# Kernel tuning notes

Hardware: AMD Instinct MI355X
Metric: run time of the kernel (lower is better)

Reference implementation:

```python
import jax, jax.numpy as jnp
import numpy as np

N_NODES = 50000


def _relgraphconv(x, W, Wloop, b, src, dst, etypes, n_nodes):
    # DGL RelGraphConv (regularizer=None, self_loop=True, norm=None):
    # out[i] = sum over incoming edges (j->i, rel r) of W_r @ x[j]  +  W_loop @ x[i]  +  b
    # low-mem form: transform all nodes per relation, then gather per edge.
    h_rel = jnp.einsum('ni,rio->rno', x, W)          # [R, N, out]
    msg = h_rel[etypes, src]                          # [E, out]
    agg = jax.ops.segment_sum(msg, dst, num_segments=n_nodes)  # [N, out]
    return agg + x @ Wloop + b


def setup_inputs() -> dict:
    key = jax.random.key(0)
    ks = jax.random.split(key, 12)
    N, E, n_state = N_NODES, 800000, 128
    inp = {
        'x': jax.random.normal(ks[0], (N, n_state), dtype=jnp.float32),
        'src': jax.random.randint(ks[1], (E,), 0, N, dtype=jnp.int32),
        'dst': jax.random.randint(ks[2], (E,), 0, N, dtype=jnp.int32),
        'etypes': jax.random.randint(ks[3], (E,), 0, 2, dtype=jnp.int32),
        'cell_size': jax.random.randint(ks[4], (N,), 0, 8, dtype=jnp.int32),
        'max_size': jax.random.randint(ks[5], (N,), 0, 8, dtype=jnp.int32),
        'W1': jax.random.normal(ks[6], (2, n_state, 64), dtype=jnp.float32) * 0.05,
        'loop1': jax.random.normal(ks[7], (n_state, 64), dtype=jnp.float32) * 0.05,
        'b1': jnp.zeros((64,), dtype=jnp.float32),
        'W2': jax.random.normal(ks[8], (2, 64, 64), dtype=jnp.float32) * 0.05,
        'loop2': jax.random.normal(ks[9], (64, 64), dtype=jnp.float32) * 0.05,
        'b2': jnp.zeros((64,), dtype=jnp.float32),
        'W3': jax.random.normal(ks[10], (2, 64, 2), dtype=jnp.float32) * 0.05,
        'loop3': jax.random.normal(ks[11], (64, 2), dtype=jnp.float32) * 0.05,
        'b3': jnp.zeros((2,), dtype=jnp.float32),
    }
    return inp


def reference(x, src, dst, etypes, cell_size, max_size,
              W1, loop1, b1, W2, loop2, b2, W3, loop3, b3):
    N = x.shape[0]
    h = jax.nn.relu(_relgraphconv(x, W1, loop1, b1, src, dst, etypes, N))
    h = jax.nn.relu(_relgraphconv(h, W2, loop2, b2, src, dst, etypes, N))
    h = _relgraphconv(h, W3, loop3, b3, src, dst, etypes, N)   # [N, 2]
    # action mask: col 0 = cannot upsize, col 1 = cannot downsize
    upper = cell_size >= (max_size - 1)
    lower = cell_size == 0
    mask = jnp.stack([upper, lower], axis=1)                   # [N, 2] bool
    return jnp.where(mask, h.min() - 1.0, h)
```

## Files before the change

kernel.cpp:

```cpp
#include <hip/hip_runtime.h>


#define STRIDE 64

typedef unsigned short ushortT;
typedef __attribute__((ext_vector_type(8))) short short8;
typedef __attribute__((ext_vector_type(4))) float f32x4;

__device__ inline ushortT f2bf(float f) {
    union { float f; unsigned u; } v; v.f = f;
    unsigned r = v.u + 0x7FFFu + ((v.u >> 16) & 1u);
    return (ushortT)(r >> 16);
}
__device__ inline float bf2f(ushortT h) {
    union { unsigned u; float f; } v; v.u = ((unsigned)h) << 16;
    return v.f;
}

__device__ inline void atomicMinF(float* addr, float v) {
    if (v >= 0.f) atomicMin((int*)addr, __float_as_int(v));
    else          atomicMax((unsigned int*)addr, __float_as_uint(v));
}

__global__ __launch_bounds__(256) void pack_scatter_kernel(
    const float* __restrict__ W1, const float* __restrict__ loop1,
    const float* __restrict__ W2, const float* __restrict__ loop2,
    ushortT* __restrict__ BP1, ushortT* __restrict__ BP2,
    const int* __restrict__ src, const int* __restrict__ dst,
    const int* __restrict__ et, int* __restrict__ cnt, int* __restrict__ eidx,
    int N, int E) {
    if (blockIdx.x < 18) {
        int g = (int)blockIdx.x * 256 + (int)threadIdx.x;
        if (g < 3072) {
            int l = g & 63, ks = (g >> 6) & 3, ct = g >> 8;
            int c = ct * 16 + (l & 15);
            int mat = c >> 6, cc = c & 63;
            int kbase = ks * 32 + (l >> 4) * 8;
            ushortT* dstp = BP1 + (size_t)g * 8;
#pragma unroll
            for (int j = 0; j < 8; ++j) {
                int k = kbase + j;
                float v = (mat < 2) ? W1[((size_t)mat * 128 + k) * 64 + cc]
                                    : loop1[(size_t)k * 64 + cc];
                dstp[j] = f2bf(v);
            }
        } else {
            int s = g - 3072;
            int l = s & 63, ks = (s >> 6) & 1, ct = s >> 7;
            int c = ct * 16 + (l & 15);
            int mat = c >> 6, cc = c & 63;
            int kbase = ks * 32 + (l >> 4) * 8;
            ushortT* dstp = BP2 + (size_t)s * 8;
#pragma unroll
            for (int j = 0; j < 8; ++j) {
                int k = kbase + j;
                float v = (mat < 2) ? W2[((size_t)mat * 64 + k) * 64 + cc]
                                    : loop2[(size_t)k * 64 + cc];
                dstp[j] = f2bf(v);
            }
        }
        return;
    }
    int e0 = ((int)blockIdx.x - 18) * 1024 + (int)threadIdx.x;
    int e1 = e0 + 256, e2 = e0 + 512, e3 = e0 + 768;
    bool a0 = e0 < E, a1 = e1 < E, a2 = e2 < E, a3 = e3 < E;
    int d0 = a0 ? dst[e0] : 0, d1 = a1 ? dst[e1] : 0;
    int d2 = a2 ? dst[e2] : 0, d3 = a3 ? dst[e3] : 0;
    int v0 = a0 ? (et[e0] * N + src[e0]) : 0;
    int v1 = a1 ? (et[e1] * N + src[e1]) : 0;
    int v2 = a2 ? (et[e2] * N + src[e2]) : 0;
    int v3 = a3 ? (et[e3] * N + src[e3]) : 0;
    int p0 = 0, p1 = 0, p2 = 0, p3 = 0;
    if (a0) p0 = atomicAdd(&cnt[d0], 1);
    if (a1) p1 = atomicAdd(&cnt[d1], 1);
    if (a2) p2 = atomicAdd(&cnt[d2], 1);
    if (a3) p3 = atomicAdd(&cnt[d3], 1);
    if (a0 && p0 < STRIDE) eidx[(size_t)d0 * STRIDE + p0] = v0;
    if (a1 && p1 < STRIDE) eidx[(size_t)d1 * STRIDE + p1] = v1;
    if (a2 && p2 < STRIDE) eidx[(size_t)d2 * STRIDE + p2] = v2;
    if (a3 && p3 < STRIDE) eidx[(size_t)d3 * STRIDE + p3] = v3;
}

__global__ __launch_bounds__(256) void gemm1_mfma(
    const float* __restrict__ x, const ushortT* __restrict__ BP1,
    const float* __restrict__ b1,
    ushortT* __restrict__ hrelb, ushortT* __restrict__ H1b, int N) {
    const int w = (int)threadIdx.x >> 6, lane = (int)threadIdx.x & 63;
    const int rowbase = ((int)blockIdx.x * 4 + w) * 16;
    const int m = lane & 15, quad = lane >> 4;
    const int nclamp = min(rowbase + m, N - 1);

    short8 a[4];
    const float* xp = x + (size_t)nclamp * 128 + quad * 8;
#pragma unroll
    for (int ks = 0; ks < 4; ++ks) {
        float4 g0 = *(const float4*)(xp + ks * 32);
        float4 g1 = *(const float4*)(xp + ks * 32 + 4);
        a[ks][0] = (short)f2bf(g0.x); a[ks][1] = (short)f2bf(g0.y);
        a[ks][2] = (short)f2bf(g0.z); a[ks][3] = (short)f2bf(g0.w);
        a[ks][4] = (short)f2bf(g1.x); a[ks][5] = (short)f2bf(g1.y);
        a[ks][6] = (short)f2bf(g1.z); a[ks][7] = (short)f2bf(g1.w);
    }

    f32x4 acc[12];
#pragma unroll
    for (int ct = 0; ct < 12; ++ct) acc[ct] = (f32x4){0.f, 0.f, 0.f, 0.f};

#pragma unroll
    for (int ks = 0; ks < 4; ++ks) {
#pragma unroll
        for (int ct = 0; ct < 12; ++ct) {
            short8 b = *(const short8*)&BP1[((size_t)(ct * 4 + ks) * 64 + lane) * 8];
            acc[ct] = __builtin_amdgcn_mfma_f32_16x16x32_bf16(a[ks], b, acc[ct], 0, 0, 0);
        }
    }

    const int node0 = rowbase + quad * 4;
#pragma unroll
    for (int ct = 0; ct < 12; ++ct) {
        int c = ct * 16 + m;
        int mat = c >> 6, cc = c & 63;
        float bias = (mat == 2) ? b1[cc] : 0.f;
#pragma unroll
        for (int j = 0; j < 4; ++j) {
            int n = node0 + j;
            if (n < N) {
                float v = acc[ct][j] + bias;
                if (mat < 2) hrelb[((size_t)mat * N + n) * 64 + cc] = f2bf(v);
                else         H1b[(size_t)n * 64 + cc] = f2bf(v);
            }
        }
    }
}

__global__ __launch_bounds__(256) void gemm2_mfma(
    const ushortT* __restrict__ H1b, const ushortT* __restrict__ BP2,
    const float* __restrict__ b2,
    ushortT* __restrict__ hrel2b, ushortT* __restrict__ H2b, int N) {
    const int w = (int)threadIdx.x >> 6, lane = (int)threadIdx.x & 63;
    const int rowbase = ((int)blockIdx.x * 4 + w) * 16;
    const int m = lane & 15, quad = lane >> 4;
    const int nclamp = min(rowbase + m, N - 1);

    short8 a[2];
    const ushortT* hp = H1b + (size_t)nclamp * 64 + quad * 8;
    a[0] = *(const short8*)(hp);
    a[1] = *(const short8*)(hp + 32);

    f32x4 acc[12];
#pragma unroll
    for (int ct = 0; ct < 12; ++ct) acc[ct] = (f32x4){0.f, 0.f, 0.f, 0.f};

#pragma unroll
    for (int ks = 0; ks < 2; ++ks) {
#pragma unroll
        for (int ct = 0; ct < 12; ++ct) {
            short8 b = *(const short8*)&BP2[((size_t)(ct * 2 + ks) * 64 + lane) * 8];
            acc[ct] = __builtin_amdgcn_mfma_f32_16x16x32_bf16(a[ks], b, acc[ct], 0, 0, 0);
        }
    }

    const int node0 = rowbase + quad * 4;
#pragma unroll
    for (int ct = 0; ct < 12; ++ct) {
        int c = ct * 16 + m;
        int mat = c >> 6, cc = c & 63;
        float bias = (mat == 2) ? b2[cc] : 0.f;
#pragma unroll
        for (int j = 0; j < 4; ++j) {
            int n = node0 + j;
            if (n < N) {
                float v = acc[ct][j] + bias;
                if (mat < 2) hrel2b[((size_t)mat * N + n) * 64 + cc] = f2bf(v);
                else         H2b[(size_t)n * 64 + cc] = f2bf(v);
            }
        }
    }
}

__global__ void agg1_kernel(const ushortT* __restrict__ hrelb, const int* __restrict__ eidx,
                            const int* __restrict__ cnt, ushortT* __restrict__ H1b, int N) {
    int node = (int)blockIdx.x * 4 + ((int)threadIdx.x >> 6);
    if (node >= N) return;
    int lane = (int)threadIdx.x & 63;
    int deg = min(cnt[node], STRIDE);
    int my = (lane < deg) ? eidx[(size_t)node * STRIDE + lane] : 0;
    float acc = bf2f(H1b[(size_t)node * 64 + lane]);
    int j = 0;
    for (; j + 7 < deg; j += 8) {
        int id[8];
        float v[8];
#pragma unroll
        for (int q = 0; q < 8; ++q) id[q] = __shfl(my, j + q, 64);
#pragma unroll
        for (int q = 0; q < 8; ++q) v[q] = bf2f(hrelb[(size_t)id[q] * 64 + lane]);
        acc += ((v[0] + v[1]) + (v[2] + v[3])) + ((v[4] + v[5]) + (v[6] + v[7]));
    }
    for (; j < deg; ++j)
        acc += bf2f(hrelb[(size_t)__shfl(my, j, 64) * 64 + lane]);
    H1b[(size_t)node * 64 + lane] = f2bf(fmaxf(acc, 0.f));
}

__global__ void k3_kernel(const ushortT* __restrict__ hrel2b, const ushortT* __restrict__ H2b,
                          const int* __restrict__ eidx, const int* __restrict__ cnt,
                          const float* __restrict__ W3, const float* __restrict__ loop3,
                          const float* __restrict__ b3,
                          float* __restrict__ hrel3, float* __restrict__ H3, int N) {
    int node = (int)blockIdx.x * 4 + ((int)threadIdx.x >> 6);
    if (node >= N) return;
    int lane = (int)threadIdx.x & 63;
    int deg = min(cnt[node], STRIDE);
    int my = (lane < deg) ? eidx[(size_t)node * STRIDE + lane] : 0;
    float acc = bf2f(H2b[(size_t)node * 64 + lane]);
    int j = 0;
    for (; j + 7 < deg; j += 8) {
        int id[8];
        float v[8];
#pragma unroll
        for (int q = 0; q < 8; ++q) id[q] = __shfl(my, j + q, 64);
#pragma unroll
        for (int q = 0; q < 8; ++q) v[q] = bf2f(hrel2b[(size_t)id[q] * 64 + lane]);
        acc += ((v[0] + v[1]) + (v[2] + v[3])) + ((v[4] + v[5]) + (v[6] + v[7]));
    }
    for (; j < deg; ++j)
        acc += bf2f(hrel2b[(size_t)__shfl(my, j, 64) * 64 + lane]);
    float xk = fmaxf(acc, 0.f);
    float p[6];
    p[0] = xk * W3[lane * 2 + 0];
    p[1] = xk * W3[lane * 2 + 1];
    p[2] = xk * W3[(64 + lane) * 2 + 0];
    p[3] = xk * W3[(64 + lane) * 2 + 1];
    p[4] = xk * loop3[lane * 2 + 0];
    p[5] = xk * loop3[lane * 2 + 1];
#pragma unroll
    for (int mm = 32; mm >= 1; mm >>= 1) {
#pragma unroll
        for (int q = 0; q < 6; ++q) p[q] += __shfl_xor(p[q], mm, 64);
    }
    if (lane == 0) {
        hrel3[(size_t)node * 2 + 0] = p[0];
        hrel3[(size_t)node * 2 + 1] = p[1];
        hrel3[((size_t)N + node) * 2 + 0] = p[2];
        hrel3[((size_t)N + node) * 2 + 1] = p[3];
        H3[(size_t)node * 2 + 0] = p[4] + b3[0];
        H3[(size_t)node * 2 + 1] = p[5] + b3[1];
    }
}

__global__ void agg3min_kernel(const float* __restrict__ hrel3, const int* __restrict__ eidx,
                               const int* __restrict__ cnt, float* __restrict__ H3,
                               float* __restrict__ minval, int N) {
    int n = (int)blockIdx.x * 256 + (int)threadIdx.x;
    float v = 3.4e38f;
    if (n < N) {
        float a0 = H3[n * 2 + 0], a1 = H3[n * 2 + 1];
        int deg = min(cnt[n], STRIDE);
        const int* row = &eidx[(size_t)n * STRIDE];
        int j = 0;
        for (; j + 3 < deg; j += 4) {
            int i0 = row[j], i1 = row[j + 1], i2 = row[j + 2], i3 = row[j + 3];
            float2 q0 = *(const float2*)&hrel3[(size_t)i0 * 2];
            float2 q1 = *(const float2*)&hrel3[(size_t)i1 * 2];
            float2 q2 = *(const float2*)&hrel3[(size_t)i2 * 2];
            float2 q3 = *(const float2*)&hrel3[(size_t)i3 * 2];
            a0 += (q0.x + q1.x) + (q2.x + q3.x);
            a1 += (q0.y + q1.y) + (q2.y + q3.y);
        }
        for (; j < deg; ++j) {
            float2 q = *(const float2*)&hrel3[(size_t)row[j] * 2];
            a0 += q.x; a1 += q.y;
        }
        H3[n * 2 + 0] = a0;
        H3[n * 2 + 1] = a1;
        v = fminf(a0, a1);
    }
#pragma unroll
    for (int mm = 32; mm >= 1; mm >>= 1) v = fminf(v, __shfl_xor(v, mm, 64));
    __shared__ float s[4];
    if ((threadIdx.x & 63) == 0) s[threadIdx.x >> 6] = v;
    __syncthreads();
    if (threadIdx.x == 0)
        atomicMinF(minval, fminf(fminf(s[0], s[1]), fminf(s[2], s[3])));
}

__global__ void mask_kernel(const float* __restrict__ H3, const float* __restrict__ minval,
                            const int* __restrict__ cs, const int* __restrict__ ms,
                            float* __restrict__ out, int N) {
    int n = (int)blockIdx.x * 256 + (int)threadIdx.x;
    if (n >= N) return;
    float m = minval[0] - 1.0f;
    bool up = cs[n] >= ms[n] - 1;
    bool lo = cs[n] == 0;
    out[n * 2 + 0] = up ? m : H3[n * 2 + 0];
    out[n * 2 + 1] = lo ? m : H3[n * 2 + 1];
}

extern "C" void kernel_launch(void* const* d_in, const int* in_sizes, int n_in,
                              void* d_out, int out_size, void* d_ws, size_t ws_size,
                              hipStream_t stream) {
    const float* x     = (const float*)d_in[0];
    const int* src     = (const int*)d_in[1];
    const int* dst     = (const int*)d_in[2];
    const int* etypes  = (const int*)d_in[3];
    const int* cellsz  = (const int*)d_in[4];
    const int* maxsz   = (const int*)d_in[5];
    const float* W1    = (const float*)d_in[6];
    const float* loop1 = (const float*)d_in[7];
    const float* b1    = (const float*)d_in[8];
    const float* W2    = (const float*)d_in[9];
    const float* loop2 = (const float*)d_in[10];
    const float* b2    = (const float*)d_in[11];
    const float* W3    = (const float*)d_in[12];
    const float* loop3 = (const float*)d_in[13];
    const float* b3    = (const float*)d_in[14];
    float* out = (float*)d_out;

    const int N = in_sizes[0] / 128;
    const int E = in_sizes[1];

    char* p = (char*)d_ws;
    auto alloc = [&](size_t bytes) -> void* {
        void* r = (void*)p;
        p += ((bytes + 255) / 256) * 256;
        return r;
    };
    ushortT* hrelb  = (ushortT*)alloc((size_t)2 * N * 64 * 2);
    ushortT* H1b    = (ushortT*)alloc((size_t)N * 64 * 2);
    ushortT* hrel2b = (ushortT*)alloc((size_t)2 * N * 64 * 2);
    ushortT* H2b    = (ushortT*)alloc((size_t)N * 64 * 2);
    float* hrel3    = (float*)alloc((size_t)2 * N * 2 * 4);
    float* H3       = (float*)alloc((size_t)N * 2 * 4);
    int* cnt        = (int*)alloc((size_t)N * 4);
    int* eidx       = (int*)alloc((size_t)N * STRIDE * 4);
    ushortT* BP1    = (ushortT*)alloc((size_t)3072 * 8 * 2);
    ushortT* BP2    = (ushortT*)alloc((size_t)1536 * 8 * 2);
    float* minval   = (float*)alloc(4);
    (void)ws_size; (void)n_in; (void)out_size;

    const int NB_N   = (N + 255) / 256;
    const int NTILES = (N + 63) / 64;
    const int NB_W   = (N + 3) / 4;
    const int NB_SC  = (E + 1023) / 1024;

    hipMemsetAsync(cnt, 0, (size_t)N * 4, stream);
    hipMemsetAsync(minval, 0x7f, 4, stream);

    pack_scatter_kernel<<<18 + NB_SC, 256, 0, stream>>>(
        W1, loop1, W2, loop2, BP1, BP2, src, dst, etypes, cnt, eidx, N, E);

    gemm1_mfma<<<NTILES, 256, 0, stream>>>(x, BP1, b1, hrelb, H1b, N);

    agg1_kernel<<<NB_W, 256, 0, stream>>>(hrelb, eidx, cnt, H1b, N);

    gemm2_mfma<<<NTILES, 256, 0, stream>>>(H1b, BP2, b2, hrel2b, H2b, N);

    k3_kernel<<<NB_W, 256, 0, stream>>>(hrel2b, H2b, eidx, cnt, W3, loop3, b3,
                                        hrel3, H3, N);

    agg3min_kernel<<<NB_N, 256, 0, stream>>>(hrel3, eidx, cnt, H3, minval, N);
    mask_kernel<<<NB_N, 256, 0, stream>>>(H3, minval, cellsz, maxsz, out, N);
}
```

Baseline: 258.0 us.

## Replace global atomic edge scatter with two-phase binned CSR build fused with GEMM1

The per-edge global atomicAdd scatter into the padded adjacency is replaced by a two-phase binning scheme. First, blocks build shared-memory histograms over 128-node destination bins, reserve space with one global atomic per bin, and write (dst, src-index) records into fixed-capacity bin buffers. These blocks run in the same launch as the first MFMA GEMM. A second kernel then builds each bin's adjacency rows with shared-memory atomics and writes clamped counts. The counter memsets are folded into the weight-packing kernel. The goal is to cut contended global atomics, localize the scattered writes, and drop launches. In exchange it adds an extra pass of bin buffer traffic, and edges are silently dropped if a bin exceeds its fixed capacity.

```diff
diff --git a/kernel.cpp b/kernel.cpp
--- a/kernel.cpp
+++ b/kernel.cpp
@@ -2,6 +2,7 @@
 
 
 #define STRIDE 64
+#define BINCAP 2560
 
 typedef unsigned short ushortT;
 typedef __attribute__((ext_vector_type(8))) short short8;
@@ -22,71 +23,91 @@
     else          atomicMax((unsigned int*)addr, __float_as_uint(v));
 }
 
-__global__ __launch_bounds__(256) void pack_scatter_kernel(
+__global__ __launch_bounds__(256) void pack_init_kernel(
     const float* __restrict__ W1, const float* __restrict__ loop1,
     const float* __restrict__ W2, const float* __restrict__ loop2,
     ushortT* __restrict__ BP1, ushortT* __restrict__ BP2,
-    const int* __restrict__ src, const int* __restrict__ dst,
-    const int* __restrict__ et, int* __restrict__ cnt, int* __restrict__ eidx,
-    int N, int E) {
-    if (blockIdx.x < 18) {
-        int g = (int)blockIdx.x * 256 + (int)threadIdx.x;
-        if (g < 3072) {
-            int l = g & 63, ks = (g >> 6) & 3, ct = g >> 8;
-            int c = ct * 16 + (l & 15);
-            int mat = c >> 6, cc = c & 63;
-            int kbase = ks * 32 + (l >> 4) * 8;
-            ushortT* dstp = BP1 + (size_t)g * 8;
-#pragma unroll
-            for (int j = 0; j < 8; ++j) {
-                int k = kbase + j;
-                float v = (mat < 2) ? W1[((size_t)mat * 128 + k) * 64 + cc]
-                                    : loop1[(size_t)k * 64 + cc];
-                dstp[j] = f2bf(v);
-            }
-        } else {
-            int s = g - 3072;
-            int l = s & 63, ks = (s >> 6) & 1, ct = s >> 7;
-            int c = ct * 16 + (l & 15);
-            int mat = c >> 6, cc = c & 63;
-            int kbase = ks * 32 + (l >> 4) * 8;
-            ushortT* dstp = BP2 + (size_t)s * 8;
-#pragma unroll
-            for (int j = 0; j < 8; ++j) {
-                int k = kbase + j;
-                float v = (mat < 2) ? W2[((size_t)mat * 64 + k) * 64 + cc]
-                                    : loop2[(size_t)k * 64 + cc];
-                dstp[j] = f2bf(v);
-            }
-        }
-        return;
-    }
-    int e0 = ((int)blockIdx.x - 18) * 1024 + (int)threadIdx.x;
-    int e1 = e0 + 256, e2 = e0 + 512, e3 = e0 + 768;
-    bool a0 = e0 < E, a1 = e1 < E, a2 = e2 < E, a3 = e3 < E;
-    int d0 = a0 ? dst[e0] : 0, d1 = a1 ? dst[e1] : 0;
-    int d2 = a2 ? dst[e2] : 0, d3 = a3 ? dst[e3] : 0;
-    int v0 = a0 ? (et[e0] * N + src[e0]) : 0;
-    int v1 = a1 ? (et[e1] * N + src[e1]) : 0;
-    int v2 = a2 ? (et[e2] * N + src[e2]) : 0;
-    int v3 = a3 ? (et[e3] * N + src[e3]) : 0;
-    int p0 = 0, p1 = 0, p2 = 0, p3 = 0;
-    if (a0) p0 = atomicAdd(&cnt[d0], 1);
-    if (a1) p1 = atomicAdd(&cnt[d1], 1);
-    if (a2) p2 = atomicAdd(&cnt[d2], 1);
-    if (a3) p3 = atomicAdd(&cnt[d3], 1);
-    if (a0 && p0 < STRIDE) eidx[(size_t)d0 * STRIDE + p0] = v0;
-    if (a1 && p1 < STRIDE) eidx[(size_t)d1 * STRIDE + p1] = v1;
-    if (a2 && p2 < STRIDE) eidx[(size_t)d2 * STRIDE + p2] = v2;
-    if (a3 && p3 < STRIDE) eidx[(size_t)d3 * STRIDE + p3] = v3;
-}
-
-__global__ __launch_bounds__(256) void gemm1_mfma(
+    int* __restrict__ bincnt, float* __restrict__ minval, int NBINS) {
+    int g = (int)blockIdx.x * 256 + (int)threadIdx.x;
+    if (g < NBINS) bincnt[g] = 0;
+    if (g == 0) *(int*)minval = 0x7f7f7f7f;
+    if (g < 3072) {
+        int l = g & 63, ks = (g >> 6) & 3, ct = g >> 8;
+        int c = ct * 16 + (l & 15);
+        int mat = c >> 6, cc = c & 63;
+        int kbase = ks * 32 + (l >> 4) * 8;
+        ushortT* dstp = BP1 + (size_t)g * 8;
+#pragma unroll
+        for (int j = 0; j < 8; ++j) {
+            int k = kbase + j;
+            float v = (mat < 2) ? W1[((size_t)mat * 128 + k) * 64 + cc]
+                                : loop1[(size_t)k * 64 + cc];
+            dstp[j] = f2bf(v);
+        }
+    } else {
+        int s = g - 3072;
+        int l = s & 63, ks = (s >> 6) & 1, ct = s >> 7;
+        int c = ct * 16 + (l & 15);
+        int mat = c >> 6, cc = c & 63;
+        int kbase = ks * 32 + (l >> 4) * 8;
+        ushortT* dstp = BP2 + (size_t)s * 8;
+#pragma unroll
+        for (int j = 0; j < 8; ++j) {
+            int k = kbase + j;
+            float v = (mat < 2) ? W2[((size_t)mat * 64 + k) * 64 + cc]
+                                : loop2[(size_t)k * 64 + cc];
+            dstp[j] = f2bf(v);
+        }
+    }
+}
+
+__global__ __launch_bounds__(256) void k1_kernel(
     const float* __restrict__ x, const ushortT* __restrict__ BP1,
     const float* __restrict__ b1,
-    ushortT* __restrict__ hrelb, ushortT* __restrict__ H1b, int N) {
-    const int w = (int)threadIdx.x >> 6, lane = (int)threadIdx.x & 63;
-    const int rowbase = ((int)blockIdx.x * 4 + w) * 16;
+    ushortT* __restrict__ hrelb, ushortT* __restrict__ H1b,
+    const int* __restrict__ src, const int* __restrict__ dst,
+    const int* __restrict__ et, int* __restrict__ bincnt, int2* __restrict__ binbuf,
+    int N, int E, int NBINS, int NBA) {
+    __shared__ int hist[512];
+    __shared__ int gbase[512];
+    __shared__ ushortT rnk[4096];
+
+    const int t = (int)threadIdx.x;
+
+    if ((int)blockIdx.x < NBA) {
+        for (int i = t; i < NBINS; i += 256) hist[i] = 0;
+        __syncthreads();
+        const int base = (int)blockIdx.x * 4096;
+#pragma unroll
+        for (int i = 0; i < 16; ++i) {
+            int e = base + t + i * 256;
+            if (e < E) {
+                int bb = dst[e] >> 7;
+                rnk[t + i * 256] = (ushortT)atomicAdd(&hist[bb], 1);
+            }
+        }
+        __syncthreads();
+        for (int i = t; i < NBINS; i += 256) {
+            int h = hist[i];
+            gbase[i] = h ? atomicAdd(&bincnt[i], h) : 0;
+        }
+        __syncthreads();
+#pragma unroll
+        for (int i = 0; i < 16; ++i) {
+            int e = base + t + i * 256;
+            if (e < E) {
+                int dd = dst[e];
+                int bb = dd >> 7;
+                int v = et[e] * N + src[e];
+                int pos = gbase[bb] + (int)rnk[t + i * 256];
+                if (pos < BINCAP)
+                    binbuf[(size_t)bb * BINCAP + pos] = make_int2(dd, v);
+            }
+        }
+        return;
+    }
+    const int w = t >> 6, lane = t & 63;
+    const int rowbase = (((int)blockIdx.x - NBA) * 4 + w) * 16;
     const int m = lane & 15, quad = lane >> 4;
     const int nclamp = min(rowbase + m, N - 1);
 
@@ -131,6 +152,49 @@
             }
         }
     }
+}
+
+__global__ __launch_bounds__(256) void phaseB_kernel(
+    const int* __restrict__ bincnt, const int2* __restrict__ binbuf,
+    int* __restrict__ cnt, int* __restrict__ eidx, int N) {
+    __shared__ int lcnt[128];
+    const int b = (int)blockIdx.x;
+    const int t = (int)threadIdx.x;
+    if (t < 128) lcnt[t] = 0;
+    __syncthreads();
+    const int cb = min(bincnt[b], BINCAP);
+    const int2* buf = binbuf + (size_t)b * BINCAP;
+    for (int i = t; i < cb; i += 256) {
+        int2 rec = buf[i];
+        int r = atomicAdd(&lcnt[rec.x & 127], 1);
+        if (r < STRIDE) eidx[(size_t)rec.x * STRIDE + r] = rec.y;
+    }
+    __syncthreads();
+    int node = b * 128 + t;
+    if (t < 128 && node < N) cnt[node] = min(lcnt[t], STRIDE);
+}
+
+__global__ void agg1_kernel(const ushortT* __restrict__ hrelb, const int* __restrict__ eidx,
+                            const int* __restrict__ cnt, ushortT* __restrict__ H1b, int N) {
+    int node = (int)blockIdx.x * 4 + ((int)threadIdx.x >> 6);
+    if (node >= N) return;
+    int lane = (int)threadIdx.x & 63;
+    int deg = cnt[node];
+    int my = (lane < deg) ? eidx[(size_t)node * STRIDE + lane] : 0;
+    float acc = bf2f(H1b[(size_t)node * 64 + lane]);
+    int j = 0;
+    for (; j + 7 < deg; j += 8) {
+        int id[8];
+        float v[8];
+#pragma unroll
+        for (int q = 0; q < 8; ++q) id[q] = __shfl(my, j + q, 64);
+#pragma unroll
+        for (int q = 0; q < 8; ++q) v[q] = bf2f(hrelb[(size_t)id[q] * 64 + lane]);
+        acc += ((v[0] + v[1]) + (v[2] + v[3])) + ((v[4] + v[5]) + (v[6] + v[7]));
+    }
+    for (; j < deg; ++j)
+        acc += bf2f(hrelb[(size_t)__shfl(my, j, 64) * 64 + lane]);
+    H1b[(size_t)node * 64 + lane] = f2bf(fmaxf(acc, 0.f));
 }
 
 __global__ __launch_bounds__(256) void gemm2_mfma(
@@ -178,29 +242,6 @@
     }
 }
 
-__global__ void agg1_kernel(const ushortT* __restrict__ hrelb, const int* __restrict__ eidx,
-                            const int* __restrict__ cnt, ushortT* __restrict__ H1b, int N) {
-    int node = (int)blockIdx.x * 4 + ((int)threadIdx.x >> 6);
-    if (node >= N) return;
-    int lane = (int)threadIdx.x & 63;
-    int deg = min(cnt[node], STRIDE);
-    int my = (lane < deg) ? eidx[(size_t)node * STRIDE + lane] : 0;
-    float acc = bf2f(H1b[(size_t)node * 64 + lane]);
-    int j = 0;
-    for (; j + 7 < deg; j += 8) {
-        int id[8];
-        float v[8];
-#pragma unroll
-        for (int q = 0; q < 8; ++q) id[q] = __shfl(my, j + q, 64);
-#pragma unroll
-        for (int q = 0; q < 8; ++q) v[q] = bf2f(hrelb[(size_t)id[q] * 64 + lane]);
-        acc += ((v[0] + v[1]) + (v[2] + v[3])) + ((v[4] + v[5]) + (v[6] + v[7]));
-    }
-    for (; j < deg; ++j)
-        acc += bf2f(hrelb[(size_t)__shfl(my, j, 64) * 64 + lane]);
-    H1b[(size_t)node * 64 + lane] = f2bf(fmaxf(acc, 0.f));
-}
-
 __global__ void k3_kernel(const ushortT* __restrict__ hrel2b, const ushortT* __restrict__ H2b,
                           const int* __restrict__ eidx, const int* __restrict__ cnt,
                           const float* __restrict__ W3, const float* __restrict__ loop3,
@@ -209,7 +250,7 @@
     int node = (int)blockIdx.x * 4 + ((int)threadIdx.x >> 6);
     if (node >= N) return;
     int lane = (int)threadIdx.x & 63;
-    int deg = min(cnt[node], STRIDE);
+    int deg = cnt[node];
     int my = (lane < deg) ? eidx[(size_t)node * STRIDE + lane] : 0;
     float acc = bf2f(H2b[(size_t)node * 64 + lane]);
     int j = 0;
@@ -254,7 +295,7 @@
     float v = 3.4e38f;
     if (n < N) {
         float a0 = H3[n * 2 + 0], a1 = H3[n * 2 + 1];
-        int deg = min(cnt[n], STRIDE);
+        int deg = cnt[n];
         const int* row = &eidx[(size_t)n * STRIDE];
         int j = 0;
         for (; j + 3 < deg; j += 4) {
@@ -335,20 +376,25 @@
     ushortT* BP1    = (ushortT*)alloc((size_t)3072 * 8 * 2);
     ushortT* BP2    = (ushortT*)alloc((size_t)1536 * 8 * 2);
     float* minval   = (float*)alloc(4);
+
+    const int NBINS = (N + 127) >> 7;
+    int* bincnt     = (int*)alloc((size_t)NBINS * 4);
+    int2* binbuf    = (int2*)alloc((size_t)NBINS * BINCAP * 8);
     (void)ws_size; (void)n_in; (void)out_size;
 
     const int NB_N   = (N + 255) / 256;
     const int NTILES = (N + 63) / 64;
     const int NB_W   = (N + 3) / 4;
-    const int NB_SC  = (E + 1023) / 1024;
-
-    hipMemsetAsync(cnt, 0, (size_t)N * 4, stream);
-    hipMemsetAsync(minval, 0x7f, 4, stream);
-
-    pack_scatter_kernel<<<18 + NB_SC, 256, 0, stream>>>(
-        W1, loop1, W2, loop2, BP1, BP2, src, dst, etypes, cnt, eidx, N, E);
-
-    gemm1_mfma<<<NTILES, 256, 0, stream>>>(x, BP1, b1, hrelb, H1b, N);
+    const int NBA    = (E + 4095) / 4096;
+
+    pack_init_kernel<<<18, 256, 0, stream>>>(
+        W1, loop1, W2, loop2, BP1, BP2, bincnt, minval, NBINS);
+
+    k1_kernel<<<NBA + NTILES, 256, 0, stream>>>(
+        x, BP1, b1, hrelb, H1b,
+        src, dst, etypes, bincnt, binbuf, N, E, NBINS, NBA);
+
+    phaseB_kernel<<<NBINS, 256, 0, stream>>>(bincnt, binbuf, cnt, eidx, N);
 
     agg1_kernel<<<NB_W, 256, 0, stream>>>(hrelb, eidx, cnt, H1b, N);
 
```

Result: faster. 218.5 us (-15.3%).
